# Performance work log

Hardware: AMD Instinct MI355X
Metric: run time of the kernel (lower is better)

The kernel has to match this reference:

```python
import jax, jax.numpy as jnp
import numpy as np

T, H, I, E, K = 4096, 2048, 1408, 8, 2  # tokens, hidden, intermediate, experts, top_k


def setup_inputs() -> dict:
    key = jax.random.key(0)
    ks = jax.random.split(key, 6)
    hidden_states = jax.random.normal(ks[0], (T, H), dtype=jnp.float32)
    gate_weight = jax.random.normal(ks[1], (E, H), dtype=jnp.float32) * 0.02  # fp32 gate, per source assert
    w13_weight = jax.random.randint(ks[2], (E, 2 * I, H), -127, 128, dtype=jnp.int8)
    w13_weight_scale = jax.random.uniform(ks[3], (E, 2 * I), dtype=jnp.float32, minval=0.5, maxval=1.5) * 0.005
    w2_weight = jax.random.randint(ks[4], (E, H, I), -127, 128, dtype=jnp.int8)
    w2_weight_scale = jax.random.uniform(ks[5], (E, H), dtype=jnp.float32, minval=0.5, maxval=1.5) * 0.005
    return dict(hidden_states=hidden_states, gate_weight=gate_weight,
                w13_weight=w13_weight, w13_weight_scale=w13_weight_scale,
                w2_weight=w2_weight, w2_weight_scale=w2_weight_scale)


def _dynamic_quant_i8(x):
    # per-token dynamic symmetric int8: scale = max|x|/127 (smooth scales default to ones)
    s = jnp.maximum(jnp.max(jnp.abs(x), axis=-1, keepdims=True) / 127.0, 1e-8)
    q = jnp.clip(jnp.round(x / s), -127.0, 127.0)
    return q, s


def reference(hidden_states, gate_weight, w13_weight, w13_weight_scale, w2_weight, w2_weight_scale):
    # --- gating: fp32 linear + topk softmax (renormalize=True) ---
    logits = hidden_states @ gate_weight.T              # [T, E]
    probs = jax.nn.softmax(logits, axis=-1)
    topv, topi = jax.lax.top_k(probs, K)                # [T, K]
    gates = topv / jnp.sum(topv, axis=-1, keepdims=True)
    # dense routing weights [T, E]: gate value where expert selected, else 0
    route = jnp.zeros((T, E), hidden_states.dtype).at[jnp.arange(T)[:, None], topi].add(gates)

    # --- dynamic per-token int8 quant of routed input (same token value for each of its K copies) ---
    q_in, s_in = _dynamic_quant_i8(hidden_states)       # [T, H], [T, 1]

    # --- grouped w8a8 GEMM (fc1) -> SwiGLU -> requant -> grouped GEMM (fc2) -> weighted combine ---
    def step(acc, xs):
        w13, s13, w2, s2w, r = xs                       # per-expert weights / route column [T]
        h1 = (q_in @ w13.T.astype(jnp.float32)) * s_in * s13[None, :]   # dequant fc1: [T, 2I]
        g, u = h1[:, :I], h1[:, I:]
        act = jax.nn.silu(g) * u                        # SwiGLU
        q_a, s_a = _dynamic_quant_i8(act)
        h2 = (q_a @ w2.T.astype(jnp.float32)) * s_a * s2w[None, :]      # dequant fc2: [T, H]
        return acc + r[:, None] * h2, None

    acc0 = jnp.zeros_like(hidden_states)
    out, _ = jax.lax.scan(step, acc0,
                          (w13_weight, w13_weight_scale, w2_weight, w2_weight_scale, route.T))
    return out
```

## Files before the change

### kernel.cpp

```cpp
#include <hip/hip_runtime.h>

#define T_TOK 4096
#define H_DIM 2048
#define I_DIM 1408
#define E_NUM 8
#define NI2   (2 * I_DIM)

typedef int v4i __attribute__((ext_vector_type(4)));

#define GLD_LDS16(gptr, lptr)                                                        \
  __builtin_amdgcn_global_load_lds(                                                  \
      (const __attribute__((address_space(1))) void*)(gptr),                         \
      (__attribute__((address_space(3))) void*)(lptr), 16, 0, 0)

__global__ __launch_bounds__(256) void pack_i8(const int* __restrict__ src,
                                               signed char* __restrict__ dst,
                                               int n16) {
  int i = blockIdx.x * 256 + threadIdx.x;
  if (i >= n16) return;
  const int4* s4 = (const int4*)src + (size_t)i * 4;
  int4 v0 = s4[0], v1 = s4[1], v2 = s4[2], v3 = s4[3];
  union { signed char c[16]; int4 v; } pk;
  pk.c[0] = (signed char)v0.x;  pk.c[1] = (signed char)v0.y;
  pk.c[2] = (signed char)v0.z;  pk.c[3] = (signed char)v0.w;
  pk.c[4] = (signed char)v1.x;  pk.c[5] = (signed char)v1.y;
  pk.c[6] = (signed char)v1.z;  pk.c[7] = (signed char)v1.w;
  pk.c[8] = (signed char)v2.x;  pk.c[9] = (signed char)v2.y;
  pk.c[10] = (signed char)v2.z; pk.c[11] = (signed char)v2.w;
  pk.c[12] = (signed char)v3.x; pk.c[13] = (signed char)v3.y;
  pk.c[14] = (signed char)v3.z; pk.c[15] = (signed char)v3.w;
  ((int4*)dst)[i] = pk.v;
}

__global__ __launch_bounds__(256) void gate_route_quant(
    const float* __restrict__ hs, const float* __restrict__ gw,
    signed char* __restrict__ qin, float* __restrict__ s_in,
    int* __restrict__ tok_list, int* __restrict__ cnt,
    int* __restrict__ epos, float* __restrict__ gts) {
  const int t = blockIdx.x;
  const int tid = threadIdx.x;
  const int lane = tid & 63;
  const int wave = tid >> 6;
  const float* row = hs + (size_t)t * H_DIM;

  const float4* r4 = (const float4*)row + tid * 2;
  float4 xa = r4[0], xb = r4[1];
  float x[8] = {xa.x, xa.y, xa.z, xa.w, xb.x, xb.y, xb.z, xb.w};

  double pd[8];
  for (int e = 0; e < 8; e++) pd[e] = 0.0;
  float am = 0.f;
  for (int j = 0; j < 8; j++) {
    float v = x[j];
    am = fmaxf(am, fabsf(v));
    int col = tid * 8 + j;
    for (int e = 0; e < 8; e++)
      pd[e] += (double)v * (double)gw[e * H_DIM + col];
  }
  for (int e = 0; e < 8; e++)
    for (int s = 32; s; s >>= 1) pd[e] += __shfl_down(pd[e], s);
  for (int s = 32; s; s >>= 1) am = fmaxf(am, __shfl_down(am, s));

  __shared__ double sred[4][8];
  __shared__ float sam[4];
  __shared__ float sbc;
  if (lane == 0) {
    for (int e = 0; e < 8; e++) sred[wave][e] = pd[e];
    sam[wave] = am;
  }
  __syncthreads();
  if (tid == 0) {
    float l[8];
    for (int e = 0; e < 8; e++)
      l[e] = (float)(sred[0][e] + sred[1][e] + sred[2][e] + sred[3][e]);
    float amx = fmaxf(fmaxf(sam[0], sam[1]), fmaxf(sam[2], sam[3]));
    float s = fmaxf(amx / 127.0f, 1e-8f);
    s_in[t] = s;
    sbc = s;
    int i1 = 0;
    for (int e = 1; e < 8; e++) if (l[e] > l[i1]) i1 = e;
    int i2 = -1;
    for (int e = 0; e < 8; e++) {
      if (e == i1) continue;
      if (i2 < 0 || l[e] > l[i2]) i2 = e;
    }
    float d = expf(l[i2] - l[i1]);
    float g1 = 1.0f / (1.0f + d);
    float g2 = d / (1.0f + d);
    int p1 = atomicAdd(&cnt[i1], 1);
    tok_list[i1 * T_TOK + p1] = t;
    int p2 = atomicAdd(&cnt[i2], 1);
    tok_list[i2 * T_TOK + p2] = t;
    epos[2 * t] = (i1 << 16) | p1;     gts[2 * t] = g1;
    epos[2 * t + 1] = (i2 << 16) | p2; gts[2 * t + 1] = g2;
  }
  __syncthreads();
  float s = sbc;
  union { signed char c[8]; unsigned long long u; } pk;
  for (int j = 0; j < 8; j++) {
    float q = rintf(x[j] / s);
    q = fminf(127.f, fmaxf(-127.f, q));
    pk.c[j] = (signed char)q;
  }
  ((unsigned long long*)(qin + (size_t)t * H_DIM))[tid] = pk.u;
}

__global__ void calc_off(const int* __restrict__ cnt, int* __restrict__ off) {
  if (threadIdx.x == 0) {
    int s = 0;
    for (int e = 0; e < E_NUM; e++) { off[e] = s; s += cnt[e]; }
  }
}

__global__ __launch_bounds__(256, 2) void gemm1_silu(
    const signed char* __restrict__ qw13, const signed char* __restrict__ qin,
    const float* __restrict__ s_in, const float* __restrict__ s13,
    const int* __restrict__ tok_list, const int* __restrict__ cnt,
    const int* __restrict__ off, float* __restrict__ act,
    unsigned int* __restrict__ amax) {
  const int e = blockIdx.z;
  const int ce = cnt[e];
  const int m0 = blockIdx.y * 128;
  if (m0 >= ce) return;
  const int n0 = blockIdx.x * 128;

  __shared__ __align__(16) signed char As[128 * 64];
  __shared__ __align__(16) signed char Bg[128 * 64];
  __shared__ __align__(16) signed char Bu[128 * 64];

  const int tid = threadIdx.x;
  const int lane = tid & 63;
  const int wave = tid >> 6;
  const int quad = lane >> 4;
  const int ln = lane & 15;
  const int wm = wave & 1;
  const int wn = wave >> 1;

  const int* tl = tok_list + e * T_TOK;
  const int rowA0 = tid >> 2;
  const int rowA1 = rowA0 + 64;
  const int kc = ((tid ^ (tid >> 4)) & 3) * 16;

  const int tA0 = tl[min(m0 + rowA0, ce - 1)];
  const int tA1 = tl[min(m0 + rowA1, ce - 1)];
  const signed char* gA0 = qin + (size_t)tA0 * H_DIM + kc;
  const signed char* gA1 = qin + (size_t)tA1 * H_DIM + kc;
  const signed char* w13e = qw13 + (size_t)e * NI2 * H_DIM;
  const signed char* gBg0 = w13e + (size_t)(n0 + rowA0) * H_DIM + kc;
  const signed char* gBg1 = w13e + (size_t)(n0 + rowA1) * H_DIM + kc;
  const signed char* gBu0 = gBg0 + (size_t)I_DIM * H_DIM;
  const signed char* gBu1 = gBg1 + (size_t)I_DIM * H_DIM;
  const int lds0 = (tid & ~63) * 16;
  const int lds1 = 4096 + lds0;

  const int rq0 = ((quad ^ (ln >> 2)) & 3) * 16;

  v4i accg[4][4], accu[4][4];
  v4i zero = {0, 0, 0, 0};
#pragma unroll
  for (int i = 0; i < 4; i++)
#pragma unroll
    for (int j = 0; j < 4; j++) { accg[i][j] = zero; accu[i][j] = zero; }

  for (int k0 = 0; k0 < H_DIM; k0 += 64) {
    __syncthreads();
    GLD_LDS16(gA0 + k0, As + lds0);
    GLD_LDS16(gA1 + k0, As + lds1);
    GLD_LDS16(gBg0 + k0, Bg + lds0);
    GLD_LDS16(gBg1 + k0, Bg + lds1);
    GLD_LDS16(gBu0 + k0, Bu + lds0);
    GLD_LDS16(gBu1 + k0, Bu + lds1);
    __syncthreads();

    v4i af[4], bgf[4], buf_[4];
#pragma unroll
    for (int mt = 0; mt < 4; mt++)
      af[mt] = *(const v4i*)(As + (wm * 64 + mt * 16 + ln) * 64 + rq0);
#pragma unroll
    for (int nt = 0; nt < 4; nt++) {
      bgf[nt] = *(const v4i*)(Bg + (wn * 64 + nt * 16 + ln) * 64 + rq0);
      buf_[nt] = *(const v4i*)(Bu + (wn * 64 + nt * 16 + ln) * 64 + rq0);
    }
#pragma unroll
    for (int mt = 0; mt < 4; mt++)
#pragma unroll
      for (int nt = 0; nt < 4; nt++) {
        accg[mt][nt] = __builtin_amdgcn_mfma_i32_16x16x64_i8(af[mt], bgf[nt], accg[mt][nt], 0, 0, 0);
        accu[mt][nt] = __builtin_amdgcn_mfma_i32_16x16x64_i8(af[mt], buf_[nt], accu[mt][nt], 0, 0, 0);
      }
  }

  const float* s13e = s13 + e * NI2;
  float sg[4], su[4];
  int ncol[4];
#pragma unroll
  for (int nt = 0; nt < 4; nt++) {
    int n = n0 + wn * 64 + nt * 16 + ln;
    ncol[nt] = n;
    sg[nt] = s13e[n];
    su[nt] = s13e[I_DIM + n];
  }
  const int offe = off[e];
#pragma unroll
  for (int mt = 0; mt < 4; mt++) {
#pragma unroll
    for (int r = 0; r < 4; r++) {
      int mrel = m0 + wm * 64 + mt * 16 + quad * 4 + r;
      bool valid = mrel < ce;
      int tok = tl[valid ? mrel : 0];
      float si = s_in[tok];
      int crow = offe + mrel;
      float* arow = act + (size_t)crow * I_DIM;
      float am = 0.f;
#pragma unroll
      for (int nt = 0; nt < 4; nt++) {
        float g = (float)accg[mt][nt][r] * si * sg[nt];
        float u = (float)accu[mt][nt][r] * si * su[nt];
        float a = g / (1.0f + expf(-g)) * u;
        if (valid) arow[ncol[nt]] = a;
        am = fmaxf(am, fabsf(a));
      }
      for (int s = 1; s < 16; s <<= 1) am = fmaxf(am, __shfl_xor(am, s, 16));
      if (valid && ln == 0) atomicMax(amax + crow, __float_as_uint(am));
    }
  }
}

__global__ __launch_bounds__(256) void quant_act(const float* __restrict__ act,
                                                 const unsigned int* __restrict__ amax,
                                                 signed char* __restrict__ qa,
                                                 float* __restrict__ s_a) {
  const int r = blockIdx.x;
  float am = __uint_as_float(amax[r]);
  float s = fmaxf(am / 127.0f, 1e-8f);
  if (threadIdx.x == 0) s_a[r] = s;
  const float* arow = act + (size_t)r * I_DIM;
  signed char* qrow = qa + (size_t)r * I_DIM;
  for (int j = threadIdx.x; j < I_DIM; j += 256) {
    float q = rintf(arow[j] / s);
    q = fminf(127.f, fmaxf(-127.f, q));
    qrow[j] = (signed char)q;
  }
}

__global__ __launch_bounds__(256, 3) void gemm2_h2(
    const signed char* __restrict__ qw2, const signed char* __restrict__ qa,
    const float* __restrict__ s_a, const float* __restrict__ s2w,
    const int* __restrict__ cnt, const int* __restrict__ off,
    float* __restrict__ h2s) {
  const int e = blockIdx.z;
  const int ce = cnt[e];
  const int m0 = blockIdx.y * 128;
  if (m0 >= ce) return;
  const int n0 = blockIdx.x * 128;
  const int offe = off[e];

  __shared__ __align__(16) signed char As[128 * 64];
  __shared__ __align__(16) signed char Bs[128 * 64];

  const int tid = threadIdx.x;
  const int lane = tid & 63;
  const int wave = tid >> 6;
  const int quad = lane >> 4;
  const int ln = lane & 15;
  const int wm = wave & 1;
  const int wn = wave >> 1;

  const int rowA0 = tid >> 2;
  const int rowA1 = rowA0 + 64;
  const int kc = ((tid ^ (tid >> 4)) & 3) * 16;

  const signed char* gA0 = qa + (size_t)(offe + min(m0 + rowA0, ce - 1)) * I_DIM + kc;
  const signed char* gA1 = qa + (size_t)(offe + min(m0 + rowA1, ce - 1)) * I_DIM + kc;
  const signed char* w2e = qw2 + (size_t)e * H_DIM * I_DIM;
  const signed char* gB0 = w2e + (size_t)(n0 + rowA0) * I_DIM + kc;
  const signed char* gB1 = w2e + (size_t)(n0 + rowA1) * I_DIM + kc;
  const int lds0 = (tid & ~63) * 16;
  const int lds1 = 4096 + lds0;
  const int rq0 = ((quad ^ (ln >> 2)) & 3) * 16;

  v4i acc[4][4];
  v4i zero = {0, 0, 0, 0};
#pragma unroll
  for (int i = 0; i < 4; i++)
#pragma unroll
    for (int j = 0; j < 4; j++) acc[i][j] = zero;

  for (int k0 = 0; k0 < I_DIM; k0 += 64) {
    __syncthreads();
    GLD_LDS16(gA0 + k0, As + lds0);
    GLD_LDS16(gA1 + k0, As + lds1);
    GLD_LDS16(gB0 + k0, Bs + lds0);
    GLD_LDS16(gB1 + k0, Bs + lds1);
    __syncthreads();

    v4i af[4], bf[4];
#pragma unroll
    for (int mt = 0; mt < 4; mt++)
      af[mt] = *(const v4i*)(As + (wm * 64 + mt * 16 + ln) * 64 + rq0);
#pragma unroll
    for (int nt = 0; nt < 4; nt++)
      bf[nt] = *(const v4i*)(Bs + (wn * 64 + nt * 16 + ln) * 64 + rq0);
#pragma unroll
    for (int mt = 0; mt < 4; mt++)
#pragma unroll
      for (int nt = 0; nt < 4; nt++)
        acc[mt][nt] = __builtin_amdgcn_mfma_i32_16x16x64_i8(af[mt], bf[nt], acc[mt][nt], 0, 0, 0);
  }

  const float* s2e = s2w + e * H_DIM;
  float sw[4];
  int ncol[4];
#pragma unroll
  for (int nt = 0; nt < 4; nt++) {
    int n = n0 + wn * 64 + nt * 16 + ln;
    ncol[nt] = n;
    sw[nt] = s2e[n];
  }
#pragma unroll
  for (int mt = 0; mt < 4; mt++) {
#pragma unroll
    for (int r = 0; r < 4; r++) {
      int mrel = m0 + wm * 64 + mt * 16 + quad * 4 + r;
      if (mrel >= ce) continue;
      float sa = s_a[offe + mrel];
      float* orow = h2s + (size_t)(offe + mrel) * H_DIM;
#pragma unroll
      for (int nt = 0; nt < 4; nt++)
        orow[ncol[nt]] = (float)acc[mt][nt][r] * sa * sw[nt];
    }
  }
}

__global__ __launch_bounds__(256) void gather_out(
    const float* __restrict__ h2s, const int* __restrict__ epos,
    const float* __restrict__ gts, const int* __restrict__ off,
    float* __restrict__ out) {
  const int t = blockIdx.x;
  int a = epos[2 * t], b = epos[2 * t + 1];
  float g1 = gts[2 * t], g2 = gts[2 * t + 1];
  int r1 = off[a >> 16] + (a & 0xffff);
  int r2 = off[b >> 16] + (b & 0xffff);
  const float4* R1 = (const float4*)(h2s + (size_t)r1 * H_DIM);
  const float4* R2 = (const float4*)(h2s + (size_t)r2 * H_DIM);
  float4* O = (float4*)(out + (size_t)t * H_DIM);
  for (int c = threadIdx.x; c < H_DIM / 4; c += 256) {
    float4 x = R1[c], y = R2[c];
    float4 z;
    z.x = g1 * x.x + g2 * y.x;
    z.y = g1 * x.y + g2 * y.y;
    z.z = g1 * x.z + g2 * y.z;
    z.w = g1 * x.w + g2 * y.w;
    O[c] = z;
  }
}

extern "C" void kernel_launch(void* const* d_in, const int* in_sizes, int n_in,
                              void* d_out, int out_size, void* d_ws, size_t ws_size,
                              hipStream_t stream) {
  const float* hs = (const float*)d_in[0];
  const float* gw = (const float*)d_in[1];
  const int* w13 = (const int*)d_in[2];
  const float* s13 = (const float*)d_in[3];
  const int* w2 = (const int*)d_in[4];
  const float* s2w = (const float*)d_in[5];
  float* out = (float*)d_out;

  char* ws = (char*)d_ws;
  size_t o = 0;
  auto take = [&](size_t b) {
    char* p = ws + o;
    o += (b + 255) & ~(size_t)255;
    return p;
  };
  signed char* qw13 = (signed char*)take((size_t)E_NUM * NI2 * H_DIM);
  signed char* qin = (signed char*)take((size_t)T_TOK * H_DIM);
  float* act = (float*)take((size_t)T_TOK * 2 * I_DIM * 4);
  float* h2s = (float*)qw13;
  signed char* qw2 = (signed char*)take((size_t)E_NUM * H_DIM * I_DIM);
  signed char* qa = (signed char*)take((size_t)T_TOK * 2 * I_DIM);
  float* sin_ = (float*)take((size_t)T_TOK * 4);
  float* sa = (float*)take((size_t)T_TOK * 2 * 4);
  unsigned int* amax = (unsigned int*)take((size_t)T_TOK * 2 * 4);
  int* tokl = (int*)take((size_t)E_NUM * T_TOK * 4);
  int* epos = (int*)take((size_t)T_TOK * 2 * 4);
  float* gts = (float*)take((size_t)T_TOK * 2 * 4);
  int* cnt = (int*)take(E_NUM * 4);
  int* off = (int*)take(E_NUM * 4);

  hipMemsetAsync(cnt, 0, E_NUM * 4, stream);
  hipMemsetAsync(amax, 0, (size_t)T_TOK * 2 * 4, stream);

  {
    int n16 = E_NUM * NI2 * H_DIM / 16;
    pack_i8<<<(n16 + 255) / 256, 256, 0, stream>>>(w13, qw13, n16);
  }
  {
    int n16 = E_NUM * H_DIM * I_DIM / 16;
    pack_i8<<<(n16 + 255) / 256, 256, 0, stream>>>(w2, qw2, n16);
  }
  gate_route_quant<<<T_TOK, 256, 0, stream>>>(hs, gw, qin, sin_, tokl, cnt, epos, gts);
  calc_off<<<1, 64, 0, stream>>>(cnt, off);
  {
    dim3 g(I_DIM / 128, T_TOK / 128, E_NUM);
    gemm1_silu<<<g, 256, 0, stream>>>(qw13, qin, sin_, s13, tokl, cnt, off, act, amax);
  }
  quant_act<<<T_TOK * 2, 256, 0, stream>>>(act, amax, qa, sa);
  {
    dim3 g(H_DIM / 128, T_TOK / 128, E_NUM);
    gemm2_h2<<<g, 256, 0, stream>>>(qw2, qa, sa, s2w, cnt, off, h2s);
  }
  gather_out<<<T_TOK, 256, 0, stream>>>(h2s, epos, gts, off, out);
}
```

Baseline: 635.2 us.

## Double-buffer LDS in both expert GEMMs and remap blocks across XCDs

Both grouped int8 GEMMs now keep two LDS stages and prefetch the next K tile with global_load_lds while computing the current one, so each iteration needs one barrier instead of two. The 3D grid is flattened into a 1D grid whose index is decoded so consecutive block ids (round-robined over the 8 XCDs) map to different M tiles that share the same expert and N tile, aiming to improve L2 reuse of weight tiles. LDS use doubles, and gemm2's launch bound drops from 3 to 2 blocks per CU, which may lower occupancy. There is no explicit vmcnt wait before the single barrier, so correctness depends on the barrier also covering completion of the async LDS loads.

```diff
diff --git a/kernel.cpp b/kernel.cpp
--- a/kernel.cpp
+++ b/kernel.cpp
@@ -118,15 +118,22 @@
     const int* __restrict__ tok_list, const int* __restrict__ cnt,
     const int* __restrict__ off, float* __restrict__ act,
     unsigned int* __restrict__ amax) {
-  const int e = blockIdx.z;
+  const int id = blockIdx.x;
+  const int xcd = id & 7;
+  const int q = id >> 3;
+  const int mhi = q & 3;
+  const int nq = (q >> 2) % 11;
+  const int e = (q >> 2) / 11;
+  const int mb = xcd + 8 * mhi;
+
   const int ce = cnt[e];
-  const int m0 = blockIdx.y * 128;
+  const int m0 = mb * 128;
   if (m0 >= ce) return;
-  const int n0 = blockIdx.x * 128;
-
-  __shared__ __align__(16) signed char As[128 * 64];
-  __shared__ __align__(16) signed char Bg[128 * 64];
-  __shared__ __align__(16) signed char Bu[128 * 64];
+  const int n0 = nq * 128;
+
+  __shared__ __align__(16) signed char As[2][128 * 64];
+  __shared__ __align__(16) signed char Bg[2][128 * 64];
+  __shared__ __align__(16) signed char Bu[2][128 * 64];
 
   const int tid = threadIdx.x;
   const int lane = tid & 63;
@@ -152,8 +159,16 @@
   const signed char* gBu1 = gBg1 + (size_t)I_DIM * H_DIM;
   const int lds0 = (tid & ~63) * 16;
   const int lds1 = 4096 + lds0;
-
   const int rq0 = ((quad ^ (ln >> 2)) & 3) * 16;
+
+  auto stage = [&](int k0, int b) {
+    GLD_LDS16(gA0 + k0, As[b] + lds0);
+    GLD_LDS16(gA1 + k0, As[b] + lds1);
+    GLD_LDS16(gBg0 + k0, Bg[b] + lds0);
+    GLD_LDS16(gBg1 + k0, Bg[b] + lds1);
+    GLD_LDS16(gBu0 + k0, Bu[b] + lds0);
+    GLD_LDS16(gBu1 + k0, Bu[b] + lds1);
+  };
 
   v4i accg[4][4], accu[4][4];
   v4i zero = {0, 0, 0, 0};
@@ -162,24 +177,21 @@
 #pragma unroll
     for (int j = 0; j < 4; j++) { accg[i][j] = zero; accu[i][j] = zero; }
 
-  for (int k0 = 0; k0 < H_DIM; k0 += 64) {
+  const int NK = H_DIM / 64;
+  stage(0, 0);
+  for (int ki = 0; ki < NK; ki++) {
     __syncthreads();
-    GLD_LDS16(gA0 + k0, As + lds0);
-    GLD_LDS16(gA1 + k0, As + lds1);
-    GLD_LDS16(gBg0 + k0, Bg + lds0);
-    GLD_LDS16(gBg1 + k0, Bg + lds1);
-    GLD_LDS16(gBu0 + k0, Bu + lds0);
-    GLD_LDS16(gBu1 + k0, Bu + lds1);
-    __syncthreads();
+    if (ki + 1 < NK) stage((ki + 1) * 64, (ki + 1) & 1);
+    const int b = ki & 1;
 
     v4i af[4], bgf[4], buf_[4];
 #pragma unroll
     for (int mt = 0; mt < 4; mt++)
-      af[mt] = *(const v4i*)(As + (wm * 64 + mt * 16 + ln) * 64 + rq0);
+      af[mt] = *(const v4i*)(As[b] + (wm * 64 + mt * 16 + ln) * 64 + rq0);
 #pragma unroll
     for (int nt = 0; nt < 4; nt++) {
-      bgf[nt] = *(const v4i*)(Bg + (wn * 64 + nt * 16 + ln) * 64 + rq0);
-      buf_[nt] = *(const v4i*)(Bu + (wn * 64 + nt * 16 + ln) * 64 + rq0);
+      bgf[nt] = *(const v4i*)(Bg[b] + (wn * 64 + nt * 16 + ln) * 64 + rq0);
+      buf_[nt] = *(const v4i*)(Bu[b] + (wn * 64 + nt * 16 + ln) * 64 + rq0);
     }
 #pragma unroll
     for (int mt = 0; mt < 4; mt++)
@@ -243,20 +255,27 @@
   }
 }
 
-__global__ __launch_bounds__(256, 3) void gemm2_h2(
+__global__ __launch_bounds__(256, 2) void gemm2_h2(
     const signed char* __restrict__ qw2, const signed char* __restrict__ qa,
     const float* __restrict__ s_a, const float* __restrict__ s2w,
     const int* __restrict__ cnt, const int* __restrict__ off,
     float* __restrict__ h2s) {
-  const int e = blockIdx.z;
+  const int id = blockIdx.x;
+  const int xcd = id & 7;
+  const int q = id >> 3;
+  const int mhi = q & 3;
+  const int nq = (q >> 2) & 15;
+  const int e = (q >> 2) >> 4;
+  const int mb = xcd + 8 * mhi;
+
   const int ce = cnt[e];
-  const int m0 = blockIdx.y * 128;
+  const int m0 = mb * 128;
   if (m0 >= ce) return;
-  const int n0 = blockIdx.x * 128;
+  const int n0 = nq * 128;
   const int offe = off[e];
 
-  __shared__ __align__(16) signed char As[128 * 64];
-  __shared__ __align__(16) signed char Bs[128 * 64];
+  __shared__ __align__(16) signed char As[2][128 * 64];
+  __shared__ __align__(16) signed char Bs[2][128 * 64];
 
   const int tid = threadIdx.x;
   const int lane = tid & 63;
@@ -279,6 +298,13 @@
   const int lds1 = 4096 + lds0;
   const int rq0 = ((quad ^ (ln >> 2)) & 3) * 16;
 
+  auto stage = [&](int k0, int b) {
+    GLD_LDS16(gA0 + k0, As[b] + lds0);
+    GLD_LDS16(gA1 + k0, As[b] + lds1);
+    GLD_LDS16(gB0 + k0, Bs[b] + lds0);
+    GLD_LDS16(gB1 + k0, Bs[b] + lds1);
+  };
+
   v4i acc[4][4];
   v4i zero = {0, 0, 0, 0};
 #pragma unroll
@@ -286,21 +312,20 @@
 #pragma unroll
     for (int j = 0; j < 4; j++) acc[i][j] = zero;
 
-  for (int k0 = 0; k0 < I_DIM; k0 += 64) {
+  const int NK = I_DIM / 64;
+  stage(0, 0);
+  for (int ki = 0; ki < NK; ki++) {
     __syncthreads();
-    GLD_LDS16(gA0 + k0, As + lds0);
-    GLD_LDS16(gA1 + k0, As + lds1);
-    GLD_LDS16(gB0 + k0, Bs + lds0);
-    GLD_LDS16(gB1 + k0, Bs + lds1);
-    __syncthreads();
+    if (ki + 1 < NK) stage((ki + 1) * 64, (ki + 1) & 1);
+    const int b = ki & 1;
 
     v4i af[4], bf[4];
 #pragma unroll
     for (int mt = 0; mt < 4; mt++)
-      af[mt] = *(const v4i*)(As + (wm * 64 + mt * 16 + ln) * 64 + rq0);
+      af[mt] = *(const v4i*)(As[b] + (wm * 64 + mt * 16 + ln) * 64 + rq0);
 #pragma unroll
     for (int nt = 0; nt < 4; nt++)
-      bf[nt] = *(const v4i*)(Bs + (wn * 64 + nt * 16 + ln) * 64 + rq0);
+      bf[nt] = *(const v4i*)(Bs[b] + (wn * 64 + nt * 16 + ln) * 64 + rq0);
 #pragma unroll
     for (int mt = 0; mt < 4; mt++)
 #pragma unroll
@@ -401,14 +426,8 @@
   }
   gate_route_quant<<<T_TOK, 256, 0, stream>>>(hs, gw, qin, sin_, tokl, cnt, epos, gts);
   calc_off<<<1, 64, 0, stream>>>(cnt, off);
-  {
-    dim3 g(I_DIM / 128, T_TOK / 128, E_NUM);
-    gemm1_silu<<<g, 256, 0, stream>>>(qw13, qin, sin_, s13, tokl, cnt, off, act, amax);
-  }
+  gemm1_silu<<<8 * 4 * 11 * 8, 256, 0, stream>>>(qw13, qin, sin_, s13, tokl, cnt, off, act, amax);
   quant_act<<<T_TOK * 2, 256, 0, stream>>>(act, amax, qa, sa);
-  {
-    dim3 g(H_DIM / 128, T_TOK / 128, E_NUM);
-    gemm2_h2<<<g, 256, 0, stream>>>(qw2, qa, sa, s2w, cnt, off, h2s);
-  }
+  gemm2_h2<<<8 * 4 * 16 * 8, 256, 0, stream>>>(qw2, qa, sa, s2w, cnt, off, h2s);
   gather_out<<<T_TOK, 256, 0, stream>>>(h2s, epos, gts, off, out);
 }
```

Measured after the change: 955.0 us. 50.3% more time.
